# Kernel optimization log

Hardware: AMD Instinct MI355X
Metric: run time of the kernel (lower is better)

## Reference

```python
import jax, jax.numpy as jnp
import numpy as np

EMB = 2048
H = 16
Q_RANK = 1536
KV_RANK = 512
ROPE_D = 64
NOPE_D = 64
V_D = 128
QK_D = ROPE_D + NOPE_D  # 128
ROPE_BASE = 10000.0
SCALING = 1.0  # query_pre_attn_scalar ** -0.5 with scalar=1.0


def apply_rope(x):
    """torchtune-style interleaved RoPE. x: (B, S, H, D)."""
    S, D = x.shape[1], x.shape[-1]
    theta = 1.0 / (ROPE_BASE ** (jnp.arange(0, D, 2, dtype=jnp.float32) / D))  # (D/2,)
    ang = jnp.arange(S, dtype=jnp.float32)[:, None] * theta[None, :]  # (S, D/2)
    cos = jnp.cos(ang)[None, :, None, :]
    sin = jnp.sin(ang)[None, :, None, :]
    xf = x.astype(jnp.float32).reshape(*x.shape[:-1], D // 2, 2)
    x0, x1 = xf[..., 0], xf[..., 1]
    out = jnp.stack([x0 * cos - x1 * sin, x1 * cos + x0 * sin], axis=-1)
    return out.reshape(x.shape).astype(x.dtype)


def setup_inputs() -> dict:
    key = jax.random.key(0)
    ks = jax.random.split(key, 6)
    s = lambda fan_in: 1.0 / np.sqrt(fan_in)
    return {
        "x": jax.random.normal(ks[0], (2, 2048, EMB), dtype=jnp.float32),
        "q_a_w": jax.random.uniform(ks[1], (Q_RANK, EMB), jnp.float32, -s(EMB), s(EMB)),
        "q_b_w": jax.random.uniform(ks[2], (H * QK_D, Q_RANK), jnp.float32, -s(Q_RANK), s(Q_RANK)),
        "kv_a_w": jax.random.uniform(ks[3], (KV_RANK + ROPE_D, EMB), jnp.float32, -s(EMB), s(EMB)),
        "kv_b_w": jax.random.uniform(ks[4], (H * (NOPE_D + V_D), KV_RANK), jnp.float32, -s(KV_RANK), s(KV_RANK)),
        "o_w": jax.random.uniform(ks[5], (EMB, H * V_D), jnp.float32, -s(H * V_D), s(H * V_D)),
    }


def reference(x, q_a_w, q_b_w, kv_a_w, kv_b_w, o_w):
    B, S, _ = x.shape
    # LoRA-compressed Q projection
    q = (x @ q_a_w.T) @ q_b_w.T  # (B, S, H*QK_D)
    q = q.reshape(B, S, H, QK_D).transpose(0, 2, 1, 3)  # (B, H, S, QK_D)
    q_pass, q_rot = q[..., :NOPE_D], q[..., NOPE_D:]
    # Compressed KV with shared rope key
    ckv = x @ kv_a_w.T  # (B, S, KV_RANK + ROPE_D)
    k_pass_c, k_rot = ckv[..., :KV_RANK], ckv[..., KV_RANK:]
    kvb = (k_pass_c @ kv_b_w.T).reshape(B, S, H, NOPE_D + V_D).transpose(0, 2, 1, 3)
    k_pass, v = kvb[..., :NOPE_D], kvb[..., NOPE_D:]  # (B,H,S,NOPE_D), (B,H,S,V_D)
    # RoPE (applied in (B,S,H,D) layout, as in the original)
    q_rot = apply_rope(q_rot.transpose(0, 2, 1, 3)).transpose(0, 2, 1, 3)
    k_rot = apply_rope(k_rot[:, :, None, :])  # (B, S, 1, ROPE_D), shared across heads
    k_rot = jnp.broadcast_to(k_rot.transpose(0, 2, 1, 3), (B, H, S, ROPE_D))
    query = jnp.concatenate([q_pass, q_rot], axis=-1)  # (B, H, S, QK_D)
    key = jnp.concatenate([k_pass, k_rot], axis=-1)
    # NOTE: original passes attention_mask=None -> no causal mask applied.
    scores = jnp.einsum("bhqd,bhkd->bhqk", query, key) * SCALING
    attn = jax.nn.softmax(scores.astype(jnp.float32), axis=-1).astype(query.dtype)
    out = jnp.einsum("bhqk,bhkd->bhqd", attn, v)  # (B, H, S, V_D)
    out = out.transpose(0, 2, 1, 3).reshape(B, S, H * V_D)
    return out @ o_w.T
```

## Files before the change

kernel.cpp:

```cpp
#include <hip/hip_runtime.h>
#include <stdint.h>

#define EMB 2048
#define NH 16
#define QRANK 1536
#define KVRANK 512
#define ROPED 64
#define NOPED 64
#define VD 128
#define QKD 128
#define SEQ 2048
#define BATCH 2
#define BS 4096
#define BHD 32
#define NCOMB 2112
#define LOG2E 1.4426950408889634f

typedef __attribute__((ext_vector_type(4))) float f32x4;
typedef __attribute__((ext_vector_type(8))) short s16x8;
typedef __attribute__((ext_vector_type(4))) short s16x4;

__device__ __forceinline__ float bf2f(unsigned short u) {
  return __uint_as_float(((unsigned int)u) << 16);
}
__device__ __forceinline__ unsigned short f2bf(float f) {
  unsigned int u = __float_as_uint(f);
  u += 0x7fff + ((u >> 16) & 1);
  return (unsigned short)(u >> 16);
}

__device__ __forceinline__ float vexp2(float x) {
#if __has_builtin(__builtin_amdgcn_exp2f)
  return __builtin_amdgcn_exp2f(x);
#else
  return exp2f(x);
#endif
}

__device__ __forceinline__ unsigned int pk_bf16_trunc(float e0, float e1) {
#if __has_builtin(__builtin_amdgcn_perm)
  return __builtin_amdgcn_perm(__float_as_uint(e1), __float_as_uint(e0), 0x07060302u);
#else
  return (__float_as_uint(e1) & 0xffff0000u) | (__float_as_uint(e0) >> 16);
#endif
}

__device__ __forceinline__ f32x4 mfma16k16(s16x4 a, s16x4 b, f32x4 c) {
#if __has_builtin(__builtin_amdgcn_mfma_f32_16x16x16_bf16)
  return __builtin_amdgcn_mfma_f32_16x16x16_bf16(a, b, c, 0, 0, 0);
#else
  return __builtin_amdgcn_mfma_f32_16x16x16bf16_1k(a, b, c, 0, 0, 0);
#endif
}

__device__ __forceinline__ void gld_lds16(const unsigned short* g, unsigned short* l) {
  __builtin_amdgcn_global_load_lds((const __attribute__((address_space(1))) void*)g,
                                   (__attribute__((address_space(3))) void*)l,
                                   16, 0, 0);
}

#define N4_X   (BS * EMB / 4)
#define N4_QA  (QRANK * EMB / 4)
#define N4_KVA ((KVRANK + ROPED) * EMB / 4)
#define N4_QB  (NH * QKD * QRANK / 4)
#define N4_KVB (NH * 192 * KVRANK / 4)
#define N4_O   (EMB * NH * VD / 4)
#define N4_TOT (N4_X + N4_QA + N4_KVA + N4_QB + N4_KVB + N4_O)

__global__ void cast_all(const float* __restrict__ x, const float* __restrict__ qa,
                         const float* __restrict__ kva, const float* __restrict__ qb,
                         const float* __restrict__ kvb, const float* __restrict__ ow,
                         unsigned short* __restrict__ Xb, unsigned short* __restrict__ Wcomb,
                         unsigned short* __restrict__ Wqb, unsigned short* __restrict__ Wkvb,
                         unsigned short* __restrict__ Wo) {
  int i = blockIdx.x * blockDim.x + threadIdx.x;
  int stride = gridDim.x * blockDim.x;
  for (; i < N4_TOT; i += stride) {
    const float4* src;
    ushort4* dst;
    int j = i;
    if (j < N4_X) { src = (const float4*)x; dst = (ushort4*)Xb; }
    else if ((j -= N4_X) < N4_QA) { src = (const float4*)qa; dst = (ushort4*)Wcomb; }
    else if ((j -= N4_QA) < N4_KVA) { src = (const float4*)kva; dst = (ushort4*)(Wcomb + (size_t)QRANK * EMB); }
    else if ((j -= N4_KVA) < N4_QB) { src = (const float4*)qb; dst = (ushort4*)Wqb; }
    else if ((j -= N4_QB) < N4_KVB) { src = (const float4*)kvb; dst = (ushort4*)Wkvb; }
    else { j -= N4_KVB; src = (const float4*)ow; dst = (ushort4*)Wo; }
    float4 v = src[j];
    ushort4 o;
    o.x = f2bf(v.x); o.y = f2bf(v.y); o.z = f2bf(v.z); o.w = f2bf(v.w);
    dst[j] = o;
  }
}

template <int OUT_F32>
__global__ __launch_bounds__(256, 2) void gemm_bt(
    const unsigned short* __restrict__ A, int lda,
    const unsigned short* __restrict__ W, int ldw,
    void* __restrict__ C, int M, int N, int K)
{
  __shared__ __align__(16) unsigned short As[128 * 64];
  __shared__ __align__(16) unsigned short Ws[128 * 64];
  const int tid = threadIdx.x;
  const int wave = tid >> 6;
  const int lane = tid & 63;
  const int ln = lane & 15;
  const int quad = lane >> 4;
  const int bm = blockIdx.y * 128;
  const int bn = blockIdx.x * 128;
  const int wm = (wave >> 1) * 64;
  const int wn = (wave & 1) * 64;

  f32x4 acc[4][4] = {};

  const int rel8 = lane >> 3;
  const int csw = ((lane & 7) ^ rel8) * 8;

  for (int k0 = 0; k0 < K; k0 += 64) {
#pragma unroll
    for (int it = 0; it < 4; ++it) {
      int rb = wave * 32 + it * 8;
      gld_lds16(A + (size_t)(bm + rb + rel8) * lda + k0 + csw, &As[rb * 64]);
    }
#pragma unroll
    for (int it = 0; it < 4; ++it) {
      int rb = wave * 32 + it * 8;
      int wr = bn + rb + rel8;
      if (wr >= N) wr = N - 1;
      gld_lds16(W + (size_t)wr * ldw + k0 + csw, &Ws[rb * 64]);
    }
    __syncthreads();
#pragma unroll
    for (int kk = 0; kk < 64; kk += 32) {
      s16x8 a[4], b[4];
#pragma unroll
      for (int mt = 0; mt < 4; ++mt)
        a[mt] = *(const s16x8*)&As[(wm + mt * 16 + ln) * 64 + ((kk / 8 + quad) ^ (ln & 7)) * 8];
#pragma unroll
      for (int nt = 0; nt < 4; ++nt)
        b[nt] = *(const s16x8*)&Ws[(wn + nt * 16 + ln) * 64 + ((kk / 8 + quad) ^ (ln & 7)) * 8];
#pragma unroll
      for (int mt = 0; mt < 4; ++mt)
#pragma unroll
        for (int nt = 0; nt < 4; ++nt)
          acc[mt][nt] = __builtin_amdgcn_mfma_f32_16x16x32_bf16(a[mt], b[nt], acc[mt][nt], 0, 0, 0);
    }
    __syncthreads();
  }
#pragma unroll
  for (int mt = 0; mt < 4; ++mt) {
    int row = bm + wm + mt * 16 + quad * 4;
#pragma unroll
    for (int nt = 0; nt < 4; ++nt) {
      int col = bn + wn + nt * 16 + ln;
      if (col < N) {
#pragma unroll
        for (int r = 0; r < 4; ++r) {
          float v = acc[mt][nt][r];
          if (OUT_F32)
            ((float*)C)[(size_t)(row + r) * N + col] = v;
          else
            ((unsigned short*)C)[(size_t)(row + r) * N + col] = f2bf(v);
        }
      }
    }
  }
}

__global__ __launch_bounds__(256, 2) void gemm_q_rope(
    const unsigned short* __restrict__ A, int lda,
    const unsigned short* __restrict__ W, int ldw,
    unsigned short* __restrict__ Qry, int K)
{
  __shared__ __align__(16) unsigned short As[128 * 64];
  __shared__ __align__(16) unsigned short Ws[128 * 64];
  const int tid = threadIdx.x;
  const int wave = tid >> 6;
  const int lane = tid & 63;
  const int ln = lane & 15;
  const int quad = lane >> 4;
  const int bm = blockIdx.y * 128;
  const int bn = blockIdx.x * 128;
  const int wm = (wave >> 1) * 64;
  const int wn = (wave & 1) * 64;

  f32x4 acc[4][4] = {};
  const int rel8 = lane >> 3;
  const int csw = ((lane & 7) ^ rel8) * 8;

  for (int k0 = 0; k0 < K; k0 += 64) {
#pragma unroll
    for (int it = 0; it < 4; ++it) {
      int rb = wave * 32 + it * 8;
      gld_lds16(A + (size_t)(bm + rb + rel8) * lda + k0 + csw, &As[rb * 64]);
    }
#pragma unroll
    for (int it = 0; it < 4; ++it) {
      int rb = wave * 32 + it * 8;
      gld_lds16(W + (size_t)(bn + rb + rel8) * ldw + k0 + csw, &Ws[rb * 64]);
    }
    __syncthreads();
#pragma unroll
    for (int kk = 0; kk < 64; kk += 32) {
      s16x8 a[4], b[4];
#pragma unroll
      for (int mt = 0; mt < 4; ++mt)
        a[mt] = *(const s16x8*)&As[(wm + mt * 16 + ln) * 64 + ((kk / 8 + quad) ^ (ln & 7)) * 8];
#pragma unroll
      for (int nt = 0; nt < 4; ++nt)
        b[nt] = *(const s16x8*)&Ws[(wn + nt * 16 + ln) * 64 + ((kk / 8 + quad) ^ (ln & 7)) * 8];
#pragma unroll
      for (int mt = 0; mt < 4; ++mt)
#pragma unroll
        for (int nt = 0; nt < 4; ++nt)
          acc[mt][nt] = __builtin_amdgcn_mfma_f32_16x16x32_bf16(a[mt], b[nt], acc[mt][nt], 0, 0, 0);
    }
    __syncthreads();
  }
  const bool odd = (ln & 1);
#pragma unroll
  for (int mt = 0; mt < 4; ++mt) {
    int rowb = bm + wm + mt * 16 + quad * 4;
#pragma unroll
    for (int nt = 0; nt < 4; ++nt) {
      int col = bn + wn + nt * 16 + ln;
      int h = col >> 7, d = col & 127;
#pragma unroll
      for (int r = 0; r < 4; ++r) {
        float v = acc[mt][nt][r];
        float other = __shfl_xor(v, 1);
        int row = rowb + r;
        int b = row >> 11, s = row & 2047;
        float y = v;
        if (d >= NOPED) {
          int i = (d - NOPED) >> 1;
          float theta = exp2f(-(float)i * (13.287712379549449f / 32.f));
          float ang = (float)s * theta;
          float sn, c;
          sincosf(ang, &sn, &c);
          y = v * c + (odd ? other * sn : -other * sn);
        }
        y *= LOG2E;
        Qry[((size_t)(b * NH + h) * SEQ + s) * QKD + d] = f2bf(y);
      }
    }
  }
}

__global__ void prep_key(const unsigned short* __restrict__ kvb,
                         const unsigned short* __restrict__ cqkv,
                         unsigned short* __restrict__ Key) {
  __shared__ unsigned short krot[ROPED];
  int bs = blockIdx.x;
  int b = bs >> 11, s = bs & 2047;
  int tid = threadIdx.x;
  if (tid < 32) {
    int i = tid;
    float x0 = bf2f(cqkv[(size_t)bs * NCOMB + QRANK + KVRANK + 2 * i]);
    float x1 = bf2f(cqkv[(size_t)bs * NCOMB + QRANK + KVRANK + 2 * i + 1]);
    float theta = exp2f(-(float)i * (13.287712379549449f / 32.f));
    float ang = (float)s * theta;
    float sn, c;
    sincosf(ang, &sn, &c);
    krot[2 * i] = f2bf(x0 * c - x1 * sn);
    krot[2 * i + 1] = f2bf(x1 * c + x0 * sn);
  }
  __syncthreads();
  for (int idx = tid; idx < NH * QKD; idx += 256) {
    int h = idx >> 7, d = idx & 127;
    unsigned short v;
    if (d < NOPED)
      v = kvb[(size_t)bs * (NH * 192) + h * 192 + d];
    else
      v = krot[d - NOPED];
    Key[((size_t)(b * NH + h) * SEQ + s) * QKD + d] = v;
  }
}

__global__ void transpose_v(const unsigned short* __restrict__ kvb, unsigned short* __restrict__ VT) {
  __shared__ unsigned short tile[64][132];
  int blk = blockIdx.x;
  int bh = blk >> 5, st = blk & 31;
  int b = bh >> 4, h = bh & 15;
  int s0 = st * 64;
  int tid = threadIdx.x;
  for (int idx = tid; idx < 64 * 128; idx += 256) {
    int sl = idx >> 7, d = idx & 127;
    tile[sl][d] = kvb[((size_t)(b * SEQ + s0 + sl)) * (NH * 192) + h * 192 + NOPED + d];
  }
  __syncthreads();
  for (int idx = tid; idx < 64 * 128; idx += 256) {
    int d = idx >> 6, sl = idx & 63;
    VT[((size_t)bh * VD + d) * SEQ + s0 + sl] = tile[sl][d];
  }
}

__global__ __launch_bounds__(256, 2) void flash_attn(
    const unsigned short* __restrict__ Q,
    const unsigned short* __restrict__ Kt,
    const unsigned short* __restrict__ VT,
    unsigned short* __restrict__ O)
{
  __shared__ __align__(16) unsigned short Ks[2][64 * 128];
  __shared__ __align__(16) unsigned short Vs[2][128 * 64];

  const int tid = threadIdx.x;
  const int wave = tid >> 6;
  const int lane = tid & 63;
  const int ln = lane & 15;
  const int quad = lane >> 4;
  const int bh = blockIdx.x;
  const int q0 = blockIdx.y * 128;
  const int b = bh >> 4, h = bh & 15;

  s16x8 qa[2][4];
#pragma unroll
  for (int mt = 0; mt < 2; ++mt) {
    const unsigned short* qrow = Q + ((size_t)bh * SEQ + q0 + wave * 32 + mt * 16 + ln) * QKD;
#pragma unroll
    for (int kx = 0; kx < 4; ++kx)
      qa[mt][kx] = *(const s16x8*)(qrow + kx * 32 + quad * 8);
  }

  const int krel = lane >> 4, kcch = lane & 15;
  const int vrel8 = lane >> 3;
  const int vc8 = (lane & 7) ^ vrel8;

  auto stage = [&](int buf, int kt) {
#pragma unroll
    for (int it = 0; it < 4; ++it) {
      int rb = wave * 16 + it * 4;
      int rr = rb + krel;
      int c = kcch ^ (rr & 15);
      gld_lds16(Kt + ((size_t)bh * SEQ + kt * 64 + rr) * QKD + c * 8, &Ks[buf][rb * 128]);
    }
#pragma unroll
    for (int it = 0; it < 4; ++it) {
      int rb = wave * 32 + it * 8;
      gld_lds16(VT + ((size_t)bh * VD + rb + vrel8) * SEQ + kt * 64 + vc8 * 8, &Vs[buf][rb * 64]);
    }
  };

  f32x4 o[2][8] = {};
  float l_i[2] = {0.f, 0.f};

  stage(0, 0);

  for (int kt = 0; kt < SEQ / 64; ++kt) {
    const int cur = kt & 1;
    if (kt + 1 < SEQ / 64) {
      stage(cur ^ 1, kt + 1);
      asm volatile("s_waitcnt vmcnt(8)" ::: "memory");
    } else {
      asm volatile("s_waitcnt vmcnt(0)" ::: "memory");
    }
    asm volatile("s_barrier" ::: "memory");

    const unsigned short* Kc = Ks[cur];
    const unsigned short* Vc = Vs[cur];

    f32x4 sc[2][4];
#pragma unroll
    for (int mt = 0; mt < 2; ++mt)
#pragma unroll
      for (int t = 0; t < 4; ++t)
        sc[mt][t] = (f32x4){-20.f, -20.f, -20.f, -20.f};
#pragma unroll
    for (int kx = 0; kx < 4; ++kx) {
      s16x8 ak[4];
#pragma unroll
      for (int t = 0; t < 4; ++t)
        ak[t] = *(const s16x8*)&Kc[(t * 16 + ln) * 128 + ((kx * 4 + quad) ^ ln) * 8];
#pragma unroll
      for (int mt = 0; mt < 2; ++mt)
#pragma unroll
        for (int t = 0; t < 4; ++t)
          sc[mt][t] = __builtin_amdgcn_mfma_f32_16x16x32_bf16(ak[t], qa[mt][kx], sc[mt][t], 0, 0, 0);
    }

    s16x4 pb[2][4];
#pragma unroll
    for (int mt = 0; mt < 2; ++mt) {
      float rs = 0.f;
#pragma unroll
      for (int t = 0; t < 4; ++t) {
        float e0 = vexp2(sc[mt][t][0]);
        float e1 = vexp2(sc[mt][t][1]);
        float e2 = vexp2(sc[mt][t][2]);
        float e3 = vexp2(sc[mt][t][3]);
        unsigned int p01 = pk_bf16_trunc(e0, e1);
        unsigned int p23 = pk_bf16_trunc(e2, e3);
        uint2 pr;
        pr.x = p01; pr.y = p23;
        pb[mt][t] = *(s16x4*)&pr;
        rs += (__uint_as_float(p01 << 16) + __uint_as_float(p01 & 0xffff0000u))
            + (__uint_as_float(p23 << 16) + __uint_as_float(p23 & 0xffff0000u));
      }
      rs += __shfl_xor(rs, 16);
      rs += __shfl_xor(rs, 32);
      l_i[mt] += rs;
    }

#pragma unroll
    for (int kc = 0; kc < 4; ++kc) {
      int gsl = ((kc * 2 + (quad >> 1)) ^ (ln & 7)) * 8 + (quad & 1) * 4;
#pragma unroll
      for (int dt = 0; dt < 8; ++dt) {
        s16x4 av = *(const s16x4*)&Vc[(dt * 16 + ln) * 64 + gsl];
#pragma unroll
        for (int mt = 0; mt < 2; ++mt)
          o[mt][dt] = mfma16k16(av, pb[mt][kc], o[mt][dt]);
      }
    }
    asm volatile("s_barrier" ::: "memory");
  }

#pragma unroll
  for (int mt = 0; mt < 2; ++mt) {
    float inv = 1.f / l_i[mt];
    int s = q0 + wave * 32 + mt * 16 + ln;
    size_t rowbase = ((size_t)b * SEQ + s) * (NH * VD) + h * VD;
#pragma unroll
    for (int dt = 0; dt < 8; ++dt) {
      ushort4 pk;
      pk.x = f2bf(o[mt][dt][0] * inv);
      pk.y = f2bf(o[mt][dt][1] * inv);
      pk.z = f2bf(o[mt][dt][2] * inv);
      pk.w = f2bf(o[mt][dt][3] * inv);
      *(ushort4*)&O[rowbase + dt * 16 + quad * 4] = pk;
    }
  }
}

extern "C" void kernel_launch(void* const* d_in, const int* in_sizes, int n_in,
                              void* d_out, int out_size, void* d_ws, size_t ws_size,
                              hipStream_t stream) {
  const float* x_f    = (const float*)d_in[0];
  const float* qaw_f  = (const float*)d_in[1];
  const float* qbw_f  = (const float*)d_in[2];
  const float* kvaw_f = (const float*)d_in[3];
  const float* kvbw_f = (const float*)d_in[4];
  const float* ow_f   = (const float*)d_in[5];

  char* ws = (char*)d_ws;
  size_t off = 0;
  auto alloc = [&](size_t n) {
    unsigned short* p = (unsigned short*)(ws + off);
    off = (off + n * 2 + 255) & ~(size_t)255;
    return p;
  };
  unsigned short* Xb    = alloc((size_t)BS * EMB);
  unsigned short* Wcomb = alloc((size_t)NCOMB * EMB);
  unsigned short* Wqb   = alloc((size_t)(NH * QKD) * QRANK);
  unsigned short* Wkvb  = alloc((size_t)(NH * 192) * KVRANK);
  unsigned short* Wo    = alloc((size_t)EMB * (NH * VD));
  unsigned short* CQKV  = alloc((size_t)BS * NCOMB);
  unsigned short* KVB   = alloc((size_t)BS * (NH * 192));
  unsigned short* Qry   = alloc((size_t)BHD * SEQ * QKD);
  unsigned short* Key   = alloc((size_t)BHD * SEQ * QKD);
  unsigned short* Vt    = alloc((size_t)BHD * VD * SEQ);
  unsigned short* AO    = alloc((size_t)BS * (NH * VD));

  cast_all<<<dim3(8192), 256, 0, stream>>>(x_f, qaw_f, kvaw_f, qbw_f, kvbw_f, ow_f,
                                           Xb, Wcomb, Wqb, Wkvb, Wo);

  gemm_bt<0><<<dim3((NCOMB + 127) / 128, BS / 128), 256, 0, stream>>>(
      Xb, EMB, Wcomb, EMB, CQKV, BS, NCOMB, EMB);
  gemm_q_rope<<<dim3((NH * QKD) / 128, BS / 128), 256, 0, stream>>>(
      CQKV, NCOMB, Wqb, QRANK, Qry, QRANK);
  gemm_bt<0><<<dim3((NH * 192) / 128, BS / 128), 256, 0, stream>>>(
      CQKV + QRANK, NCOMB, Wkvb, KVRANK, KVB, BS, NH * 192, KVRANK);

  prep_key<<<dim3(BS), 256, 0, stream>>>(KVB, CQKV, Key);
  transpose_v<<<dim3(BHD * (SEQ / 64)), 256, 0, stream>>>(KVB, Vt);

  flash_attn<<<dim3(BHD, SEQ / 128), 256, 0, stream>>>(Qry, Key, Vt, AO);

  gemm_bt<1><<<dim3(EMB / 128, BS / 128), 256, 0, stream>>>(
      AO, NH * VD, Wo, NH * VD, d_out, BS, EMB, NH * VD);
}
```

Measured before the change: 387.0 us.

## Use 16x16x32 MFMA for PV via permlane-swapped P fragments and set wave priority

Replaces the 16x16x16 bf16 MFMAs in the P·V product with 16x16x32 MFMAs. The P fragments are rearranged in registers with v_permlane32/16_swap so each lane holds 8 contiguous keys, and V is read as 16-byte LDS vectors. This halves the MFMA instruction count and the number of LDS reads for V. It also raises wave priority around the MFMA sections with s_setprio to help overlap across waves. The correctness of the key ordering depends on the permlane shuffle matching the swizzled V layout.

Measured after the change: 385.7 us. About the same (-0.3%).

```diff
diff --git a/kernel.cpp b/kernel.cpp
--- a/kernel.cpp
+++ b/kernel.cpp
@@ -19,6 +19,7 @@
 typedef __attribute__((ext_vector_type(4))) float f32x4;
 typedef __attribute__((ext_vector_type(8))) short s16x8;
 typedef __attribute__((ext_vector_type(4))) short s16x4;
+typedef __attribute__((ext_vector_type(2))) unsigned int u32x2;
 
 __device__ __forceinline__ float bf2f(unsigned short u) {
   return __uint_as_float(((unsigned int)u) << 16);
@@ -45,11 +46,20 @@
 #endif
 }
 
-__device__ __forceinline__ f32x4 mfma16k16(s16x4 a, s16x4 b, f32x4 c) {
-#if __has_builtin(__builtin_amdgcn_mfma_f32_16x16x16_bf16)
-  return __builtin_amdgcn_mfma_f32_16x16x16_bf16(a, b, c, 0, 0, 0);
+__device__ __forceinline__ void pl32swap(unsigned int& a, unsigned int& b) {
+#if __has_builtin(__builtin_amdgcn_permlane32_swap)
+  u32x2 r = __builtin_amdgcn_permlane32_swap(a, b, false, false);
+  a = r.x; b = r.y;
 #else
-  return __builtin_amdgcn_mfma_f32_16x16x16bf16_1k(a, b, c, 0, 0, 0);
+  asm("v_permlane32_swap_b32 %0, %1" : "+v"(a), "+v"(b));
+#endif
+}
+__device__ __forceinline__ void pl16swap(unsigned int& a, unsigned int& b) {
+#if __has_builtin(__builtin_amdgcn_permlane16_swap)
+  u32x2 r = __builtin_amdgcn_permlane16_swap(a, b, false, false);
+  a = r.x; b = r.y;
+#else
+  asm("v_permlane16_swap_b32 %0, %1" : "+v"(a), "+v"(b));
 #endif
 }
 
@@ -364,6 +374,7 @@
 #pragma unroll
       for (int t = 0; t < 4; ++t)
         sc[mt][t] = (f32x4){-20.f, -20.f, -20.f, -20.f};
+    __builtin_amdgcn_s_setprio(1);
 #pragma unroll
     for (int kx = 0; kx < 4; ++kx) {
       s16x8 ak[4];
@@ -376,11 +387,13 @@
         for (int t = 0; t < 4; ++t)
           sc[mt][t] = __builtin_amdgcn_mfma_f32_16x16x32_bf16(ak[t], qa[mt][kx], sc[mt][t], 0, 0, 0);
     }
-
-    s16x4 pb[2][4];
+    __builtin_amdgcn_s_setprio(0);
+
+    s16x8 pfrag[2][2];
 #pragma unroll
     for (int mt = 0; mt < 2; ++mt) {
       float rs = 0.f;
+      unsigned int pw[4][2];
 #pragma unroll
       for (int t = 0; t < 4; ++t) {
         float e0 = vexp2(sc[mt][t][0]);
@@ -389,28 +402,40 @@
         float e3 = vexp2(sc[mt][t][3]);
         unsigned int p01 = pk_bf16_trunc(e0, e1);
         unsigned int p23 = pk_bf16_trunc(e2, e3);
-        uint2 pr;
-        pr.x = p01; pr.y = p23;
-        pb[mt][t] = *(s16x4*)&pr;
+        pw[t][0] = p01; pw[t][1] = p23;
         rs += (__uint_as_float(p01 << 16) + __uint_as_float(p01 & 0xffff0000u))
             + (__uint_as_float(p23 << 16) + __uint_as_float(p23 & 0xffff0000u));
       }
       rs += __shfl_xor(rs, 16);
       rs += __shfl_xor(rs, 32);
       l_i[mt] += rs;
-    }
-
-#pragma unroll
-    for (int kc = 0; kc < 4; ++kc) {
-      int gsl = ((kc * 2 + (quad >> 1)) ^ (ln & 7)) * 8 + (quad & 1) * 4;
-#pragma unroll
-      for (int dt = 0; dt < 8; ++dt) {
-        s16x4 av = *(const s16x4*)&Vc[(dt * 16 + ln) * 64 + gsl];
-#pragma unroll
-        for (int mt = 0; mt < 2; ++mt)
-          o[mt][dt] = mfma16k16(av, pb[mt][kc], o[mt][dt]);
+#pragma unroll
+      for (int W = 0; W < 2; ++W) {
+        unsigned int u0 = pw[2 * W][0], v0 = pw[2 * W + 1][0];
+        unsigned int u1 = pw[2 * W][1], v1 = pw[2 * W + 1][1];
+        pl32swap(u0, v0); pl16swap(u0, v0);
+        pl32swap(u1, v1); pl16swap(u1, v1);
+        union { unsigned int u[4]; s16x8 v; } fb;
+        fb.u[0] = u0;
+        fb.u[1] = u1;
+        fb.u[2] = v0;
+        fb.u[3] = v1;
+        pfrag[mt][W] = fb.v;
       }
     }
+
+    __builtin_amdgcn_s_setprio(1);
+#pragma unroll
+    for (int dt = 0; dt < 8; ++dt) {
+      s16x8 av0 = *(const s16x8*)&Vc[(dt * 16 + ln) * 64 + ((quad ^ (ln & 7)) * 8)];
+      s16x8 av1 = *(const s16x8*)&Vc[(dt * 16 + ln) * 64 + (((4 + quad) ^ (ln & 7)) * 8)];
+#pragma unroll
+      for (int mt = 0; mt < 2; ++mt) {
+        o[mt][dt] = __builtin_amdgcn_mfma_f32_16x16x32_bf16(av0, pfrag[mt][0], o[mt][dt], 0, 0, 0);
+        o[mt][dt] = __builtin_amdgcn_mfma_f32_16x16x32_bf16(av1, pfrag[mt][1], o[mt][dt], 0, 0, 0);
+      }
+    }
+    __builtin_amdgcn_s_setprio(0);
     asm volatile("s_barrier" ::: "memory");
   }
 
```
